# Performance work log

Hardware: AMD Instinct MI355X
Metric: run time of the kernel (lower is better)

The kernel has to match this reference:

```python
import jax, jax.numpy as jnp
import numpy as np

NUM_HEADS = 8

def setup_inputs() -> dict:
    key = jax.random.key(0)
    ks = jax.random.split(key, 5)
    B, L, D = 4, 2048, 512
    return {
        "query": jax.random.normal(ks[0], (B, L, D), jnp.float32),
        "key":   jax.random.normal(ks[1], (B, L, D), jnp.float32),
        "value": jax.random.normal(ks[2], (B, L, D), jnp.float32),
        "w_out": jax.random.normal(ks[3], (D, D), jnp.float32) * (1.0 / np.sqrt(D)),
        "b_out": jnp.zeros((D,), jnp.float32),
    }

def _scatter_rows(base, idx, vals):
    # base: [L, ...], idx: [u], vals: [u, ...]
    return base.at[idx].set(vals)

_scatter_bh = jax.vmap(jax.vmap(_scatter_rows))  # over (B, H)

def reference(query, key, value, w_out, b_out):
    B, L, D = query.shape
    H = NUM_HEADS
    hd = D // H
    scale = 1.0 / np.sqrt(hd)

    def split(x):
        return x.reshape(B, L, H, hd).transpose(0, 2, 1, 3)  # [B,H,L,hd]
    q, k, v = split(query), split(key), split(value)

    # dense scores for sparsity measure
    scores = jnp.einsum('bhld,bhmd->bhlm', q, k) * scale  # [B,H,L,L]
    m1 = jax.scipy.special.logsumexp(scores, axis=-1) - np.log(L).astype(np.float32)
    m2 = scores.mean(axis=-1)
    M_measure = m1 - m2  # [B,H,L]

    u = max(1, int(np.ceil(np.log(L + 1))))
    _, topk_idx = jax.lax.top_k(M_measure, u)  # [B,H,u]

    v_avg = v.mean(axis=2, keepdims=True)  # [B,H,1,hd]
    default_output = jnp.broadcast_to(v_avg, (B, H, L, hd))

    q_active = jnp.take_along_axis(q, topk_idx[..., None], axis=2)  # [B,H,u,hd]
    scores_active = jnp.einsum('bhud,bhmd->bhum', q_active, k) * scale  # [B,H,u,L]
    attn_weights_active = jax.nn.softmax(scores_active, axis=-1)  # dropout p=0
    attn_output_active = jnp.einsum('bhum,bhmd->bhud', attn_weights_active, v)  # [B,H,u,hd]

    attn_output = _scatter_bh(default_output, topk_idx, attn_output_active)  # [B,H,L,hd]
    attn_weights_full = _scatter_bh(
        jnp.zeros((B, H, L, L), scores.dtype), topk_idx, attn_weights_active)

    out = attn_output.transpose(0, 2, 1, 3).reshape(B, L, D)
    out = out @ w_out.T + b_out
    return out, attn_weights_full
```

## Files before the change

### kernel.cpp

```cpp
#include <hip/hip_runtime.h>
#include <hip/hip_bf16.h>

#define BB 4
#define LL 2048
#define DD 512
#define HH 8
#define HD 64
#define UU 8
#define BH (BB*HH)
#define SCALE 0.125f
#define ASCALE 0.18033688011112042f

typedef __attribute__((ext_vector_type(8))) short short8;
typedef __attribute__((ext_vector_type(4))) float f32x4;
typedef unsigned short ushortT;

#define GLDS(gp, lp) __builtin_amdgcn_global_load_lds( \
    (const __attribute__((address_space(1))) void*)(gp), \
    (__attribute__((address_space(3))) void*)(lp), 16, 0, 0)

__device__ __forceinline__ unsigned short bf16_rne(float x) {
    unsigned int u = __float_as_uint(x);
    unsigned int r = u + 0x7FFFu + ((u >> 16) & 1u);
    return (unsigned short)(r >> 16);
}

__global__ __launch_bounds__(256) void prep(const float* __restrict__ Kin,
                                            const float* __restrict__ Vin,
                                            float* __restrict__ vsum_part,
                                            float* __restrict__ ksum_part,
                                            ushortT* __restrict__ KhiG,
                                            int* __restrict__ map) {
    int t = threadIdx.x;
    if (blockIdx.x < 256) {
        int blk = blockIdx.x;
        if (blk < 32) map[blk*256 + t] = 0;
        int bh = blk & 31, chunk = blk >> 5;
        int b = bh / HH, h = bh % HH;
        int d = t & 63; int g = t >> 6;
        const float* kb = Kin + (size_t)b*LL*DD + h*HD + d;
        const float* vb = Vin + (size_t)b*LL*DD + h*HD + d;
        float ak = 0.f, av = 0.f;
        for (int l = chunk*256 + g; l < chunk*256 + 256; l += 4) {
            ak += kb[(size_t)l*DD]; av += vb[(size_t)l*DD];
        }
        __shared__ float sk[4][64], sv[4][64];
        sk[g][d] = ak; sv[g][d] = av;
        __syncthreads();
        if (g == 0) {
            ksum_part[chunk*2048 + bh*64 + d] = sk[0][d]+sk[1][d]+sk[2][d]+sk[3][d];
            vsum_part[chunk*2048 + bh*64 + d] = sv[0][d]+sv[1][d]+sv[2][d]+sv[3][d];
        }
        return;
    }
    int blk = blockIdx.x - 256;
    int bh = blk >> 5, tile = blk & 31;
    int b = bh / HH, h = bh % HH;
    const float* kb = Kin + (size_t)b*LL*DD + h*HD;
    #pragma unroll
    for (int i = 0; i < 4; i++) {
        int f = t + i*256;
        int row = f >> 4, col4 = f & 15;
        float4 kv = *(const float4*)(kb + (size_t)(tile*64 + row)*DD + col4*4);
        float xs[4] = {kv.x, kv.y, kv.z, kv.w};
        unsigned short hb[4];
        #pragma unroll
        for (int j = 0; j < 4; j++) hb[j] = bf16_rne(xs[j]);
        int off = row*64 + (((col4>>1) ^ (row&7))<<3) + (col4&1)*4;
        uint2 uh; uh.x = hb[0] | ((unsigned)hb[1]<<16); uh.y = hb[2] | ((unsigned)hb[3]<<16);
        *(uint2*)&KhiG[(size_t)blk*4096 + off] = uh;
    }
}

__global__ __launch_bounds__(256) void m_mfma(const float* __restrict__ Q,
                                              const ushortT* __restrict__ KhiG,
                                              const float* __restrict__ ksum_part,
                                              float* __restrict__ M) {
    int qt = blockIdx.x;
    int bh = blockIdx.y; int b = bh / HH, h = bh % HH;
    const int t = threadIdx.x;
    const int lane = t & 63, w = t >> 6;
    const int c = lane & 15, G = lane >> 4;

    __shared__ unsigned short kHi[2][4096];
    __shared__ float ksLds[64];
    __shared__ float sm[128];

    const float* qb = Q + (size_t)b*LL*DD + h*HD;
    const char* khg = (const char*)(KhiG + (size_t)bh*32*4096);

    short8 a_hi[2][2], a_lo[2][2];
    #pragma unroll
    for (int g = 0; g < 2; g++) {
        int qrow = qt*128 + w*32 + g*16 + c;
        const float* qr = qb + (size_t)qrow*DD + G*8;
        #pragma unroll
        for (int dh = 0; dh < 2; dh++) {
            float4 x0 = *(const float4*)(qr + dh*32);
            float4 x1 = *(const float4*)(qr + dh*32 + 4);
            float x[8] = {x0.x,x0.y,x0.z,x0.w, x1.x,x1.y,x1.z,x1.w};
            short8 hi, lo;
            #pragma unroll
            for (int j = 0; j < 8; j++) {
                float xs = x[j] * ASCALE;
                unsigned short hb = bf16_rne(xs);
                float hf = __uint_as_float((unsigned int)hb << 16);
                hi[j] = (short)hb;
                lo[j] = (short)bf16_rne(xs - hf);
            }
            a_hi[g][dh] = hi; a_lo[g][dh] = lo;
        }
    }
    if (t < 64) {
        float s = 0.f;
        #pragma unroll
        for (int cc = 0; cc < 8; cc++) s += ksum_part[cc*2048 + bh*64 + t];
        ksLds[t] = s;
    }

    {
        char* dH = (char*)&kHi[0][0];
        unsigned o0 = w*1024, o1 = w*1024 + 4096;
        GLDS(khg + o0 + lane*16, dH + o0);
        GLDS(khg + o1 + lane*16, dH + o1);
    }
    float se[2][4] = {};
    __syncthreads();

    for (int r = 0; r < 32; r++) {
        int p = r & 1;
        if (r < 31) {
            const char* sH = khg + (size_t)(r+1)*8192;
            char* dH = (char*)&kHi[p^1][0];
            unsigned o0 = w*1024, o1 = w*1024 + 4096;
            GLDS(sH + o0 + lane*16, dH + o0);
            GLDS(sH + o1 + lane*16, dH + o1);
        }
        #pragma unroll
        for (int kt = 0; kt < 4; kt++) {
            int rowIn = kt*16 + c;
            int sw = rowIn & 7;
            int base = rowIn*64;
            short8 bh0 = *(const short8*)&kHi[p][base + ((G       ^ sw)<<3)];
            short8 bh1 = *(const short8*)&kHi[p][base + (((G + 4) ^ sw)<<3)];
            #pragma unroll
            for (int g = 0; g < 2; g++) {
                f32x4 acc = {0.f, 0.f, 0.f, 0.f};
                acc = __builtin_amdgcn_mfma_f32_16x16x32_bf16(a_hi[g][0], bh0, acc, 0, 0, 0);
                acc = __builtin_amdgcn_mfma_f32_16x16x32_bf16(a_hi[g][1], bh1, acc, 0, 0, 0);
                acc = __builtin_amdgcn_mfma_f32_16x16x32_bf16(a_lo[g][0], bh0, acc, 0, 0, 0);
                acc = __builtin_amdgcn_mfma_f32_16x16x32_bf16(a_lo[g][1], bh1, acc, 0, 0, 0);
                #pragma unroll
                for (int q4 = 0; q4 < 4; q4++) se[g][q4] += exp2f(acc[q4]);
            }
        }
        __syncthreads();
    }

    #pragma unroll
    for (int g = 0; g < 2; g++)
        #pragma unroll
        for (int q4 = 0; q4 < 4; q4++) {
            float v = se[g][q4];
            v += __shfl_xor(v, 1);
            v += __shfl_xor(v, 2);
            v += __shfl_xor(v, 4);
            v += __shfl_xor(v, 8);
            se[g][q4] = v;
        }
    if (c == 0) {
        #pragma unroll
        for (int g = 0; g < 2; g++)
            #pragma unroll
            for (int q4 = 0; q4 < 4; q4++)
                sm[w*32 + g*16 + G*4 + q4] = se[g][q4];
    }
    __syncthreads();
    if (t < 128) {
        int qrow = qt*128 + t;
        const float* qr = qb + (size_t)qrow*DD;
        float dot = 0.f;
        for (int d0 = 0; d0 < 64; d0 += 4) {
            float4 qv = *(const float4*)(qr + d0);
            dot += qv.x*ksLds[d0] + qv.y*ksLds[d0+1] + qv.z*ksLds[d0+2] + qv.w*ksLds[d0+3];
        }
        M[bh*LL + qrow] = __logf(sm[t]) - __logf((float)LL) - dot * (SCALE/(float)LL);
    }
}

__global__ __launch_bounds__(256) void top8(const float* __restrict__ M,
                                            int* __restrict__ idx,
                                            int* __restrict__ map) {
    int bh = blockIdx.x; int t = threadIdx.x;
    __shared__ float Ml[LL];
    __shared__ float vals[256];
    __shared__ int   vidx[256];
    for (int i = t; i < LL; i += 256) Ml[i] = M[bh*LL + i];
    __syncthreads();
    for (int r = 0; r < UU; r++) {
        float bv = -1e30f; int bi = 0;
        for (int i = t; i < LL; i += 256) {
            float v = Ml[i];
            if (v > bv) { bv = v; bi = i; }
        }
        vals[t] = bv; vidx[t] = bi;
        __syncthreads();
        for (int s = 128; s > 0; s >>= 1) {
            if (t < s) {
                if (vals[t+s] > vals[t] ||
                    (vals[t+s] == vals[t] && vidx[t+s] < vidx[t])) {
                    vals[t] = vals[t+s]; vidx[t] = vidx[t+s];
                }
            }
            __syncthreads();
        }
        if (t == 0) {
            int w = vidx[0];
            idx[bh*UU + r] = w;
            Ml[w] = -1e30f;
            atomicOr(&map[(bh/HH)*LL + w], 1 << (bh % HH));
        }
        __syncthreads();
    }
}

__global__ __launch_bounds__(256) void active_attn(const float* __restrict__ Q,
                                                   const float* __restrict__ Kin,
                                                   const float* __restrict__ Vin,
                                                   const int* __restrict__ idx,
                                                   const float* __restrict__ vsum_part,
                                                   const float* __restrict__ w_out,
                                                   const float* __restrict__ b_out,
                                                   float* __restrict__ attn_o,
                                                   float* __restrict__ defo,
                                                   float* __restrict__ Wfull) {
    __shared__ float qs[64];
    __shared__ float w[LL];
    __shared__ float red[256];
    __shared__ float Kt[256][65];
    __shared__ float red4[16][16][4];
    int t = threadIdx.x;
    if (blockIdx.x >= BH*UU) {
        int b = blockIdx.x - BH*UU;
        for (int i = t; i < DD; i += 256) {
            float s = 0.f;
            #pragma unroll
            for (int cc = 0; cc < 8; cc++)
                s += vsum_part[cc*2048 + (b*HH + (i >> 6))*64 + (i & 63)];
            w[i] = s * (1.0f/LL);
        }
        __syncthreads();
        for (int dp = t; dp < DD; dp += 256) {
            const float* wr = w_out + (size_t)dp*DD;
            float acc = b_out[dp];
            for (int d0 = 0; d0 < DD; d0 += 4) {
                float4 wv = *(const float4*)(wr + d0);
                acc += w[d0]*wv.x + w[d0+1]*wv.y + w[d0+2]*wv.z + w[d0+3]*wv.w;
            }
            defo[b*DD + dp] = acc;
        }
        return;
    }
    int e = blockIdx.x;
    int bh = e / UU;
    int b = bh / HH, h = bh % HH;
    int l = idx[e];
    if (t < 64) qs[t] = Q[(size_t)b*LL*DD + (size_t)l*DD + h*HD + t];
    const float* kb = Kin + (size_t)b*LL*DD + h*HD;
    int srow = t >> 4, scol = t & 15;
    float4 nx[16];
    #pragma unroll
    for (int i = 0; i < 16; i++)
        nx[i] = *(const float4*)(kb + (size_t)(srow + i*16)*DD + scol*4);
    #pragma unroll
    for (int i = 0; i < 16; i++)
        *(float4*)&Kt[srow + i*16][scol*4] = nx[i];
    __syncthreads();

    float s[8];
    float mx = -1e30f;
    #pragma unroll
    for (int p = 0; p < 8; p++) {
        if (p < 7) {
            #pragma unroll
            for (int i = 0; i < 16; i++)
                nx[i] = *(const float4*)(kb + (size_t)((p+1)*256 + srow + i*16)*DD + scol*4);
        }
        float acc = 0.f;
        for (int d0 = 0; d0 < 64; d0 += 4) {
            acc += qs[d0]*Kt[t][d0] + qs[d0+1]*Kt[t][d0+1]
                 + qs[d0+2]*Kt[t][d0+2] + qs[d0+3]*Kt[t][d0+3];
        }
        s[p] = acc * SCALE;
        mx = fmaxf(mx, s[p]);
        __syncthreads();
        if (p < 7) {
            #pragma unroll
            for (int i = 0; i < 16; i++)
                *(float4*)&Kt[srow + i*16][scol*4] = nx[i];
        }
        __syncthreads();
    }
    red[t] = mx; __syncthreads();
    for (int st = 128; st > 0; st >>= 1) { if (t < st) red[t] = fmaxf(red[t], red[t+st]); __syncthreads(); }
    mx = red[0]; __syncthreads();
    float lsum = 0.f;
    #pragma unroll
    for (int p = 0; p < 8; p++) { s[p] = __expf(s[p] - mx); lsum += s[p]; }
    red[t] = lsum; __syncthreads();
    for (int st = 128; st > 0; st >>= 1) { if (t < st) red[t] += red[t+st]; __syncthreads(); }
    float inv = 1.0f / red[0]; __syncthreads();
    float* wrow = Wfull + ((size_t)bh*LL + l) * LL;
    #pragma unroll
    for (int p = 0; p < 8; p++) {
        int m = (p << 8) + t;
        float wn = s[p] * inv;
        w[m] = wn;
        wrow[m] = wn;
    }
    __syncthreads();
    const float4* vb4 = (const float4*)(Vin + (size_t)b*LL*DD + h*HD);
    int grp = t >> 4, d4 = t & 15;
    f32x4 acc = {0.f, 0.f, 0.f, 0.f};
    for (int it = 0; it < 128; it++) {
        int m = grp + it*16;
        float4 v4 = vb4[(size_t)m*128 + d4];
        float wm = w[m];
        acc[0] += wm * v4.x; acc[1] += wm * v4.y;
        acc[2] += wm * v4.z; acc[3] += wm * v4.w;
    }
    *(f32x4*)&red4[grp][d4][0] = acc;
    __syncthreads();
    if (t < 64) {
        int dq = t >> 2, comp = t & 3;
        float sum = 0.f;
        #pragma unroll
        for (int g = 0; g < 16; g++) sum += red4[g][dq][comp];
        attn_o[e*64 + t] = sum;
    }
}

__global__ __launch_bounds__(256) void out_kernel(const float* __restrict__ defo,
                                                  const float* __restrict__ vsum_part,
                                                  const float* __restrict__ attn_o,
                                                  const int* __restrict__ idx,
                                                  const int* __restrict__ map,
                                                  const float* __restrict__ w_out,
                                                  const float* __restrict__ b_out,
                                                  float* __restrict__ out,
                                                  float* __restrict__ Wfull) {
    int l = blockIdx.x, b = blockIdx.y;
    int t = threadIdx.x;

    {
        int fid = b*LL + l;
        f32x4* Wz = (f32x4*)Wfull;
        const f32x4 z = {0.f, 0.f, 0.f, 0.f};
        #pragma unroll
        for (int rr = 0; rr < 8; rr++) {
            int R = fid*8 + rr;
            int bh2 = R >> 11, l2 = R & 2047;
            int b2 = bh2 >> 3, h2 = bh2 & 7;
            if (!((map[b2*LL + l2] >> h2) & 1)) {
                f32x4* rowp = Wz + (size_t)R*512;
                rowp[t] = z;
                rowp[t + 256] = z;
            }
        }
    }

    float* orow = out + ((size_t)b*LL + l) * DD;
    int mp = map[b*LL + l];
    if (mp == 0) {
        const float* dr = defo + b*DD;
        orow[t] = dr[t]; orow[t + 256] = dr[t + 256];
        return;
    }
    __shared__ float x[DD];
    for (int i = t; i < DD; i += 256) {
        float s = 0.f;
        #pragma unroll
        for (int cc = 0; cc < 8; cc++)
            s += vsum_part[cc*2048 + (b*HH + (i >> 6))*64 + (i & 63)];
        x[i] = s * (1.0f/LL);
    }
    __syncthreads();
    if (t < 64) {
        for (int h = 0; h < HH; h++) if (mp & (1 << h)) {
            int bh = b*HH + h;
            int e = bh*UU;
            for (int j = 0; j < UU; j++) if (idx[bh*UU + j] == l) { e = bh*UU + j; break; }
            x[h*64 + t] = attn_o[e*64 + t];
        }
    }
    __syncthreads();
    for (int dp = t; dp < DD; dp += 256) {
        const float* wr = w_out + (size_t)dp*DD;
        float acc = b_out[dp];
        for (int d0 = 0; d0 < DD; d0 += 4) {
            float4 wv = *(const float4*)(wr + d0);
            acc += x[d0]*wv.x + x[d0+1]*wv.y + x[d0+2]*wv.z + x[d0+3]*wv.w;
        }
        orow[dp] = acc;
    }
}

extern "C" void kernel_launch(void* const* d_in, const int* in_sizes, int n_in,
                              void* d_out, int out_size, void* d_ws, size_t ws_size,
                              hipStream_t stream) {
    const float* Q     = (const float*)d_in[0];
    const float* Kin   = (const float*)d_in[1];
    const float* Vin   = (const float*)d_in[2];
    const float* w_out = (const float*)d_in[3];
    const float* b_out = (const float*)d_in[4];

    float* out   = (float*)d_out;
    float* Wfull = out + (size_t)BB*LL*DD;

    char* ws = (char*)d_ws;
    float*   vsum_part = (float*)(ws);
    float*   ksum_part = (float*)(ws + 65536);
    float*   M         = (float*)(ws + 131072);
    int*     idx       = (int*)  (ws + 393216);
    float*   attn_o    = (float*)(ws + 394240);
    int*     map       = (int*)  (ws + 459776);
    float*   defo      = (float*)(ws + 493568);
    ushortT* KhiG      = (ushortT*)(ws + (1u<<20));

    prep<<<1280, 256, 0, stream>>>(Kin, Vin, vsum_part, ksum_part, KhiG, map);
    m_mfma<<<dim3(16, BH), 256, 0, stream>>>(Q, KhiG, ksum_part, M);
    top8<<<BH, 256, 0, stream>>>(M, idx, map);
    active_attn<<<BH*UU + BB, 256, 0, stream>>>(Q, Kin, Vin, idx, vsum_part, w_out, b_out,
                                                attn_o, defo, Wfull);
    out_kernel<<<dim3(LL, BB), 256, 0, stream>>>(defo, vsum_part, attn_o, idx, map,
                                                 w_out, b_out, out, Wfull);
}
```

Before: 370.2 us.

## Fuse active-row attention into output kernel and merge defo into top-k

Removes the separate active_attn kernel. Each output block whose row was selected by any head now computes that head's softmax attention inline, then does the projection. The default-output projection moves into the top-k kernel as extra blocks, which drops the idx and attn_o buffers and one launch. The inline path reads K rows with per-thread strided loads instead of staging them through LDS, so memory access may be less efficient.

```diff
diff --git a/kernel.cpp b/kernel.cpp
--- a/kernel.cpp
+++ b/kernel.cpp
@@ -188,13 +188,38 @@
     }
 }
 
-__global__ __launch_bounds__(256) void top8(const float* __restrict__ M,
-                                            int* __restrict__ idx,
-                                            int* __restrict__ map) {
-    int bh = blockIdx.x; int t = threadIdx.x;
+__global__ __launch_bounds__(256) void top8_defo(const float* __restrict__ M,
+                                                 const float* __restrict__ vsum_part,
+                                                 const float* __restrict__ w_out,
+                                                 const float* __restrict__ b_out,
+                                                 int* __restrict__ map,
+                                                 float* __restrict__ defo) {
+    int t = threadIdx.x;
     __shared__ float Ml[LL];
     __shared__ float vals[256];
     __shared__ int   vidx[256];
+    if (blockIdx.x >= BH) {
+        int b = blockIdx.x - BH;
+        for (int i = t; i < DD; i += 256) {
+            float s = 0.f;
+            #pragma unroll
+            for (int cc = 0; cc < 8; cc++)
+                s += vsum_part[cc*2048 + (b*HH + (i >> 6))*64 + (i & 63)];
+            Ml[i] = s * (1.0f/LL);
+        }
+        __syncthreads();
+        for (int dp = t; dp < DD; dp += 256) {
+            const float* wr = w_out + (size_t)dp*DD;
+            float acc = b_out[dp];
+            for (int d0 = 0; d0 < DD; d0 += 4) {
+                float4 wv = *(const float4*)(wr + d0);
+                acc += Ml[d0]*wv.x + Ml[d0+1]*wv.y + Ml[d0+2]*wv.z + Ml[d0+3]*wv.w;
+            }
+            defo[b*DD + dp] = acc;
+        }
+        return;
+    }
+    int bh = blockIdx.x;
     for (int i = t; i < LL; i += 256) Ml[i] = M[bh*LL + i];
     __syncthreads();
     for (int r = 0; r < UU; r++) {
@@ -216,7 +241,6 @@
         }
         if (t == 0) {
             int w = vidx[0];
-            idx[bh*UU + r] = w;
             Ml[w] = -1e30f;
             atomicOr(&map[(bh/HH)*LL + w], 1 << (bh % HH));
         }
@@ -224,131 +248,16 @@
     }
 }
 
-__global__ __launch_bounds__(256) void active_attn(const float* __restrict__ Q,
-                                                   const float* __restrict__ Kin,
-                                                   const float* __restrict__ Vin,
-                                                   const int* __restrict__ idx,
-                                                   const float* __restrict__ vsum_part,
-                                                   const float* __restrict__ w_out,
-                                                   const float* __restrict__ b_out,
-                                                   float* __restrict__ attn_o,
-                                                   float* __restrict__ defo,
-                                                   float* __restrict__ Wfull) {
-    __shared__ float qs[64];
-    __shared__ float w[LL];
-    __shared__ float red[256];
-    __shared__ float Kt[256][65];
-    __shared__ float red4[16][16][4];
-    int t = threadIdx.x;
-    if (blockIdx.x >= BH*UU) {
-        int b = blockIdx.x - BH*UU;
-        for (int i = t; i < DD; i += 256) {
-            float s = 0.f;
-            #pragma unroll
-            for (int cc = 0; cc < 8; cc++)
-                s += vsum_part[cc*2048 + (b*HH + (i >> 6))*64 + (i & 63)];
-            w[i] = s * (1.0f/LL);
-        }
-        __syncthreads();
-        for (int dp = t; dp < DD; dp += 256) {
-            const float* wr = w_out + (size_t)dp*DD;
-            float acc = b_out[dp];
-            for (int d0 = 0; d0 < DD; d0 += 4) {
-                float4 wv = *(const float4*)(wr + d0);
-                acc += w[d0]*wv.x + w[d0+1]*wv.y + w[d0+2]*wv.z + w[d0+3]*wv.w;
-            }
-            defo[b*DD + dp] = acc;
-        }
-        return;
-    }
-    int e = blockIdx.x;
-    int bh = e / UU;
-    int b = bh / HH, h = bh % HH;
-    int l = idx[e];
-    if (t < 64) qs[t] = Q[(size_t)b*LL*DD + (size_t)l*DD + h*HD + t];
-    const float* kb = Kin + (size_t)b*LL*DD + h*HD;
-    int srow = t >> 4, scol = t & 15;
-    float4 nx[16];
-    #pragma unroll
-    for (int i = 0; i < 16; i++)
-        nx[i] = *(const float4*)(kb + (size_t)(srow + i*16)*DD + scol*4);
-    #pragma unroll
-    for (int i = 0; i < 16; i++)
-        *(float4*)&Kt[srow + i*16][scol*4] = nx[i];
-    __syncthreads();
-
-    float s[8];
-    float mx = -1e30f;
-    #pragma unroll
-    for (int p = 0; p < 8; p++) {
-        if (p < 7) {
-            #pragma unroll
-            for (int i = 0; i < 16; i++)
-                nx[i] = *(const float4*)(kb + (size_t)((p+1)*256 + srow + i*16)*DD + scol*4);
-        }
-        float acc = 0.f;
-        for (int d0 = 0; d0 < 64; d0 += 4) {
-            acc += qs[d0]*Kt[t][d0] + qs[d0+1]*Kt[t][d0+1]
-                 + qs[d0+2]*Kt[t][d0+2] + qs[d0+3]*Kt[t][d0+3];
-        }
-        s[p] = acc * SCALE;
-        mx = fmaxf(mx, s[p]);
-        __syncthreads();
-        if (p < 7) {
-            #pragma unroll
-            for (int i = 0; i < 16; i++)
-                *(float4*)&Kt[srow + i*16][scol*4] = nx[i];
-        }
-        __syncthreads();
-    }
-    red[t] = mx; __syncthreads();
-    for (int st = 128; st > 0; st >>= 1) { if (t < st) red[t] = fmaxf(red[t], red[t+st]); __syncthreads(); }
-    mx = red[0]; __syncthreads();
-    float lsum = 0.f;
-    #pragma unroll
-    for (int p = 0; p < 8; p++) { s[p] = __expf(s[p] - mx); lsum += s[p]; }
-    red[t] = lsum; __syncthreads();
-    for (int st = 128; st > 0; st >>= 1) { if (t < st) red[t] += red[t+st]; __syncthreads(); }
-    float inv = 1.0f / red[0]; __syncthreads();
-    float* wrow = Wfull + ((size_t)bh*LL + l) * LL;
-    #pragma unroll
-    for (int p = 0; p < 8; p++) {
-        int m = (p << 8) + t;
-        float wn = s[p] * inv;
-        w[m] = wn;
-        wrow[m] = wn;
-    }
-    __syncthreads();
-    const float4* vb4 = (const float4*)(Vin + (size_t)b*LL*DD + h*HD);
-    int grp = t >> 4, d4 = t & 15;
-    f32x4 acc = {0.f, 0.f, 0.f, 0.f};
-    for (int it = 0; it < 128; it++) {
-        int m = grp + it*16;
-        float4 v4 = vb4[(size_t)m*128 + d4];
-        float wm = w[m];
-        acc[0] += wm * v4.x; acc[1] += wm * v4.y;
-        acc[2] += wm * v4.z; acc[3] += wm * v4.w;
-    }
-    *(f32x4*)&red4[grp][d4][0] = acc;
-    __syncthreads();
-    if (t < 64) {
-        int dq = t >> 2, comp = t & 3;
-        float sum = 0.f;
-        #pragma unroll
-        for (int g = 0; g < 16; g++) sum += red4[g][dq][comp];
-        attn_o[e*64 + t] = sum;
-    }
-}
-
-__global__ __launch_bounds__(256) void out_kernel(const float* __restrict__ defo,
-                                                  const float* __restrict__ vsum_part,
-                                                  const float* __restrict__ attn_o,
-                                                  const int* __restrict__ idx,
-                                                  const int* __restrict__ map,
-                                                  const float* __restrict__ w_out,
-                                                  const float* __restrict__ b_out,
-                                                  float* __restrict__ out,
-                                                  float* __restrict__ Wfull) {
+__global__ __launch_bounds__(256) void out_mega(const float* __restrict__ Q,
+                                                const float* __restrict__ Kin,
+                                                const float* __restrict__ Vin,
+                                                const float* __restrict__ defo,
+                                                const float* __restrict__ vsum_part,
+                                                const int* __restrict__ map,
+                                                const float* __restrict__ w_out,
+                                                const float* __restrict__ b_out,
+                                                float* __restrict__ out,
+                                                float* __restrict__ Wfull) {
     int l = blockIdx.x, b = blockIdx.y;
     int t = threadIdx.x;
 
@@ -376,7 +285,12 @@
         orow[t] = dr[t]; orow[t + 256] = dr[t + 256];
         return;
     }
+
     __shared__ float x[DD];
+    __shared__ float qs[64];
+    __shared__ float w[LL];
+    __shared__ float red[256];
+    __shared__ float red4[16][16][4];
     for (int i = t; i < DD; i += 256) {
         float s = 0.f;
         #pragma unroll
@@ -385,15 +299,66 @@
         x[i] = s * (1.0f/LL);
     }
     __syncthreads();
-    if (t < 64) {
-        for (int h = 0; h < HH; h++) if (mp & (1 << h)) {
-            int bh = b*HH + h;
-            int e = bh*UU;
-            for (int j = 0; j < UU; j++) if (idx[bh*UU + j] == l) { e = bh*UU + j; break; }
-            x[h*64 + t] = attn_o[e*64 + t];
-        }
-    }
-    __syncthreads();
+
+    for (int h = 0; h < HH; h++) if (mp & (1 << h)) {
+        int bh = b*HH + h;
+        if (t < 64) qs[t] = Q[(size_t)b*LL*DD + (size_t)l*DD + h*HD + t];
+        __syncthreads();
+        const float* kb = Kin + (size_t)b*LL*DD + h*HD;
+        float s[8];
+        float mx = -1e30f;
+        #pragma unroll
+        for (int p = 0; p < 8; p++) {
+            int m = t + p*256;
+            const float* kr = kb + (size_t)m*DD;
+            float acc = 0.f;
+            for (int d0 = 0; d0 < 64; d0 += 4) {
+                float4 kv = *(const float4*)(kr + d0);
+                acc += qs[d0]*kv.x + qs[d0+1]*kv.y + qs[d0+2]*kv.z + qs[d0+3]*kv.w;
+            }
+            s[p] = acc * SCALE;
+            mx = fmaxf(mx, s[p]);
+        }
+        red[t] = mx; __syncthreads();
+        for (int st = 128; st > 0; st >>= 1) { if (t < st) red[t] = fmaxf(red[t], red[t+st]); __syncthreads(); }
+        mx = red[0]; __syncthreads();
+        float lsum = 0.f;
+        #pragma unroll
+        for (int p = 0; p < 8; p++) { s[p] = __expf(s[p] - mx); lsum += s[p]; }
+        red[t] = lsum; __syncthreads();
+        for (int st = 128; st > 0; st >>= 1) { if (t < st) red[t] += red[t+st]; __syncthreads(); }
+        float inv = 1.0f / red[0]; __syncthreads();
+        float* wrow = Wfull + ((size_t)bh*LL + l) * LL;
+        #pragma unroll
+        for (int p = 0; p < 8; p++) {
+            int m = (p << 8) + t;
+            float wn = s[p] * inv;
+            w[m] = wn;
+            wrow[m] = wn;
+        }
+        __syncthreads();
+        const float4* vb4 = (const float4*)(Vin + (size_t)b*LL*DD + h*HD);
+        int grp = t >> 4, d4 = t & 15;
+        f32x4 acc4 = {0.f, 0.f, 0.f, 0.f};
+        for (int it = 0; it < 128; it++) {
+            int m = grp + it*16;
+            float4 v4 = vb4[(size_t)m*128 + d4];
+            float wm = w[m];
+            acc4[0] += wm * v4.x; acc4[1] += wm * v4.y;
+            acc4[2] += wm * v4.z; acc4[3] += wm * v4.w;
+        }
+        *(f32x4*)&red4[grp][d4][0] = acc4;
+        __syncthreads();
+        if (t < 64) {
+            int dq = t >> 2, comp = t & 3;
+            float sum = 0.f;
+            #pragma unroll
+            for (int g = 0; g < 16; g++) sum += red4[g][dq][comp];
+            x[h*64 + t] = sum;
+        }
+        __syncthreads();
+    }
+
     for (int dp = t; dp < DD; dp += 256) {
         const float* wr = w_out + (size_t)dp*DD;
         float acc = b_out[dp];
@@ -421,17 +386,13 @@
     float*   vsum_part = (float*)(ws);
     float*   ksum_part = (float*)(ws + 65536);
     float*   M         = (float*)(ws + 131072);
-    int*     idx       = (int*)  (ws + 393216);
-    float*   attn_o    = (float*)(ws + 394240);
-    int*     map       = (int*)  (ws + 459776);
-    float*   defo      = (float*)(ws + 493568);
+    int*     map       = (int*)  (ws + 393216);
+    float*   defo      = (float*)(ws + 425984);
     ushortT* KhiG      = (ushortT*)(ws + (1u<<20));
 
     prep<<<1280, 256, 0, stream>>>(Kin, Vin, vsum_part, ksum_part, KhiG, map);
     m_mfma<<<dim3(16, BH), 256, 0, stream>>>(Q, KhiG, ksum_part, M);
-    top8<<<BH, 256, 0, stream>>>(M, idx, map);
-    active_attn<<<BH*UU + BB, 256, 0, stream>>>(Q, Kin, Vin, idx, vsum_part, w_out, b_out,
-                                                attn_o, defo, Wfull);
-    out_kernel<<<dim3(LL, BB), 256, 0, stream>>>(defo, vsum_part, attn_o, idx, map,
-                                                 w_out, b_out, out, Wfull);
-}
+    top8_defo<<<BH + BB, 256, 0, stream>>>(M, vsum_part, w_out, b_out, map, defo);
+    out_mega<<<dim3(LL, BB), 256, 0, stream>>>(Q, Kin, Vin, defo, vsum_part, map,
+                                               w_out, b_out, out, Wfull);
+}
```

Result: faster. 347.7 us, median of 3 (-6.1%).
